# Kernel tuning notes

Measured on AMD Instinct MI355X. Metric: run time of the kernel, lower is better.

## Reference

```python
import jax, jax.numpy as jnp
import numpy as np

B, C, W, H = 4, 256, 64, 64
N = W * H
SCALE = 0.02  # keep QK^T energies in a stable softmax range


def setup_inputs() -> dict:
    key = jax.random.key(0)
    ks = jax.random.split(key, 8)
    return {
        "x": jax.random.normal(ks[0], (B, C, W, H), jnp.float32),
        "geo_embed": jax.random.normal(ks[1], (B, N, C), jnp.float32),
        "Wq": jax.random.normal(ks[2], (C, C), jnp.float32) * SCALE,
        "bq": jnp.zeros((C,), jnp.float32),
        "Wk": jax.random.normal(ks[3], (C, C), jnp.float32) * SCALE,
        "bk": jnp.zeros((C,), jnp.float32),
        "Wv": jax.random.normal(ks[4], (C, C), jnp.float32) * SCALE,
        "bv": jnp.zeros((C,), jnp.float32),
        "Wgp": jax.random.normal(ks[5], (C, C), jnp.float32) * SCALE,
        "bgp": jnp.zeros((C,), jnp.float32),
        "Wgg": jax.random.normal(ks[6], (1, 2 * C), jnp.float32) * SCALE,
        "bgg": jnp.zeros((1,), jnp.float32),
    }


def reference(x, geo_embed, Wq, bq, Wk, bk, Wv, bv, Wgp, bgp, Wgg, bgg):
    b, c, w, h = x.shape
    n = w * h
    xf = x.reshape(b, c, n)  # [B, C, N]

    # 1x1 conv == per-pixel linear; q laid out [B, N, O] (permuted in torch)
    q = jnp.einsum("oc,bcn->bno", Wq, xf) + bq  # [B, N, O]

    # geo gating on the query
    ge = geo_embed @ Wgp.T + bgp  # [B, N, O]
    gate = jax.nn.sigmoid(jnp.concatenate([q, ge], axis=-1) @ Wgg.T + bgg)  # [B, N, 1]
    q = q + gate * ge

    k = jnp.einsum("oc,bcn->bon", Wk, xf) + bk[:, None]  # [B, O, N]
    v = jnp.einsum("oc,bcn->bon", Wv, xf) + bv[:, None]  # [B, C, N]

    energy = jnp.einsum("bno,bom->bnm", q, k)  # [B, N, N]
    attention = jax.nn.softmax(energy, axis=-1)

    # out = bmm(value, attention^T): out[b,c,m] = sum_n v[b,c,n] * attention[b,m,n]
    out = jnp.einsum("bcn,bmn->bcm", v, attention).reshape(b, c, w, h)

    # output gating: torch .view reinterpretation of (B, N, O) as (B, C, W, H)
    ge_r = ge.reshape(b, c, w, h)
    out = out * (1.0 + jax.nn.sigmoid(ge_r))
    return out, attention
```

## Files before the change

kernel.cpp:

```cpp
#include <hip/hip_runtime.h>
#include <hip/hip_bf16.h>
#include <math.h>

static constexpr int BB = 4;
static constexpr int CC = 256;
static constexpr int NN = 4096;

using bf16   = __bf16;
using f16    = _Float16;
using bf16x8 = __attribute__((ext_vector_type(8))) __bf16;
using bf16x4 = __attribute__((ext_vector_type(4))) __bf16;
using f16x8  = __attribute__((ext_vector_type(8))) _Float16;
using f32x4  = __attribute__((ext_vector_type(4))) float;

__device__ inline void gload_lds16(const void* g, void* l) {
  __builtin_amdgcn_global_load_lds(
      (const __attribute__((address_space(1))) void*)g,
      (__attribute__((address_space(3))) void*)l, 16, 0, 0);
}

__device__ inline void swz_bid(int& xb, int& yb, int& zb) {
  int gx = gridDim.x, gy = gridDim.y;
  int nwg = gx * gy * (int)gridDim.z;
  int flat = blockIdx.x + gx * (blockIdx.y + gy * blockIdx.z);
  int q = nwg >> 3;
  int w = (flat & 7) * q + (flat >> 3);
  xb = w % gx;
  int r = w / gx;
  yb = r % gy;
  zb = r / gy;
}

__global__ __launch_bounds__(256) void cvt_weights_kernel(
    const float* __restrict__ w0, const float* __restrict__ w1,
    const float* __restrict__ w2, const float* __restrict__ w3,
    bf16* __restrict__ out) {
  const float* srcs[4] = {w0, w1, w2, w3};
  const float* s = srcs[blockIdx.y];
  bf16* dst = out + (size_t)blockIdx.y * (CC * CC);
  int i = (blockIdx.x * 256 + threadIdx.x) * 4;
  float4 v = *(const float4*)(s + i);
  bf16x4 t;
  t[0] = (bf16)v.x; t[1] = (bf16)v.y; t[2] = (bf16)v.z; t[3] = (bf16)v.w;
  *(bf16x4*)(dst + i) = t;
}

__global__ __launch_bounds__(256) void cvt_f32_bf16_kernel(
    const float* __restrict__ in, bf16* __restrict__ out, long n) {
  long i = ((long)blockIdx.x * blockDim.x + threadIdx.x) * 4;
  if (i >= n) return;
  float4 v = *(const float4*)(in + i);
  bf16x4 t;
  t[0] = (bf16)v.x; t[1] = (bf16)v.y; t[2] = (bf16)v.z; t[3] = (bf16)v.w;
  *(bf16x4*)(out + i) = t;
}

__global__ __launch_bounds__(256) void transpose_x_kernel(
    const float* __restrict__ x, bf16* __restrict__ xt) {
  __shared__ float tile[64][65];
  int b  = blockIdx.z;
  int c0 = blockIdx.x * 64;
  int n0 = blockIdx.y * 64;
  const float* xp = x  + (long)b * CC * NN;
  bf16*       xtp = xt + (long)b * NN * CC;
  int tj = threadIdx.x & 63;
  int ti = threadIdx.x >> 6;
#pragma unroll
  for (int p = 0; p < 16; ++p) {
    int i = ti + p * 4;
    tile[i][tj] = xp[(long)(c0 + i) * NN + n0 + tj];
  }
  __syncthreads();
#pragma unroll
  for (int p = 0; p < 16; ++p) {
    int i = ti + p * 4;
    xtp[(long)(n0 + i) * CC + c0 + tj] = (bf16)tile[tj][i];
  }
}

__global__ __launch_bounds__(256) void proj_all_kernel(
    const bf16* __restrict__ xt, const bf16* __restrict__ geob,
    const bf16* __restrict__ Wall,
    const float* __restrict__ bq, const float* __restrict__ bgp,
    const float* __restrict__ bk, const float* __restrict__ bv,
    bf16* __restrict__ qn, float* __restrict__ ge,
    bf16* __restrict__ kn, bf16* __restrict__ vb) {
  __shared__ bf16 As[128 * 32];
  __shared__ bf16 Bs[128 * 32];
  const long NCst = (long)NN * CC;
  const int bz = blockIdx.z;
  const int b = bz >> 2, p = bz & 3;
  const bf16 *Ap, *Bp;
  const float* bias;
  int row0, col0;
  if (p == 3) {
    Ap = Wall + 2 * CC * CC;
    Bp = xt + b * NCst;
    bias = bv;
    row0 = blockIdx.x * 128;
    col0 = blockIdx.y * 128;
  } else {
    Ap = (p == 1 ? geob : xt) + b * NCst;
    Bp = Wall + (size_t)(p == 0 ? 0 : (p == 1 ? 3 : 1)) * CC * CC;
    bias = (p == 0 ? bq : (p == 1 ? bgp : bk));
    row0 = blockIdx.y * 128;
    col0 = blockIdx.x * 128;
  }

  const int t   = threadIdx.x;
  const int wid = t >> 6;
  const int l   = t & 63;
  const int lr  = l & 15;
  const int lk  = (l >> 4) * 8;
  const int warow = (wid >> 1) * 64;
  const int wbcol = (wid & 1) * 64;
  const int srow = t >> 2;
  const int scol = (t & 3) * 8;

  f32x4 acc[4][4];
#pragma unroll
  for (int i = 0; i < 4; ++i)
#pragma unroll
    for (int j = 0; j < 4; ++j) acc[i][j] = {0.f, 0.f, 0.f, 0.f};

  for (int k0 = 0; k0 < CC; k0 += 32) {
    __syncthreads();
#pragma unroll
    for (int q = 0; q < 2; ++q)
      gload_lds16(Ap + (long)(row0 + srow + 64 * q) * CC + k0 + scol,
                  As + ((q * 256 + t) * 8));
#pragma unroll
    for (int q = 0; q < 2; ++q)
      gload_lds16(Bp + (long)(col0 + srow + 64 * q) * CC + k0 + scol,
                  Bs + ((q * 256 + t) * 8));
    __syncthreads();
    bf16x8 a[4], bb[4];
#pragma unroll
    for (int i = 0; i < 4; ++i)
      a[i] = *(const bf16x8*)(As + (warow + 16 * i + lr) * 32 + lk);
#pragma unroll
    for (int j = 0; j < 4; ++j)
      bb[j] = *(const bf16x8*)(Bs + (wbcol + 16 * j + lr) * 32 + lk);
#pragma unroll
    for (int i = 0; i < 4; ++i)
#pragma unroll
      for (int j = 0; j < 4; ++j)
        acc[i][j] = __builtin_amdgcn_mfma_f32_16x16x32_bf16(a[i], bb[j], acc[i][j], 0, 0, 0);
  }

  const int orow = (l >> 4) * 4;
  const int ocol = l & 15;
#pragma unroll
  for (int i = 0; i < 4; ++i) {
#pragma unroll
    for (int j = 0; j < 4; ++j) {
      int colb = col0 + wbcol + 16 * j + ocol;
#pragma unroll
      for (int r = 0; r < 4; ++r) {
        int row = row0 + warow + 16 * i + orow + r;
        if (p == 3) {
          float vv = acc[i][j][r] + bias[row];
          vb[b * NCst + (long)row * NN + colb] = (bf16)vv;
        } else {
          float vv = acc[i][j][r] + bias[colb];
          long di = b * NCst + (long)row * CC + colb;
          if (p == 1)
            ge[di] = vv;
          else
            (p == 0 ? qn : kn)[di] = (bf16)vv;
        }
      }
    }
  }
}

template <int BIAS_MODE, int B_MODE, int OUT_MODE, bool GATE_EPI, bool SWZ, bool STAT>
__global__ __launch_bounds__(256) void gemm_nt_lds(
    const bf16* __restrict__ A, const void* __restrict__ Bm,
    const float* __restrict__ bias, void* __restrict__ D,
    const float* __restrict__ gefl, float2* __restrict__ pstat,
    int Ncols, int K, long sA, long sB, long sD, long sGe) {
  __shared__ bf16 As[128 * 32];
  __shared__ bf16 Bs[128 * 32];
  int bx = blockIdx.x, by = blockIdx.y, bz = blockIdx.z;
  if constexpr (SWZ) swz_bid(bx, by, bz);
  const bf16* Ab = A + (long)bz * sA;
  const float* geb = GATE_EPI ? (gefl + bz * sGe) : nullptr;

  const int t   = threadIdx.x;
  const int wid = t >> 6;
  const int l   = t & 63;
  const int lr  = l & 15;
  const int lk  = (l >> 4) * 8;
  const int row0 = by * 128;
  const int col0 = bx * 128;
  const int warow = (wid >> 1) * 64;
  const int wbcol = (wid & 1) * 64;

  const int srow = t >> 2;
  const int scol = (t & 3) * 8;
  const int frow = t >> 3;
  const int fc4  = (t & 7) * 4;

  f32x4 acc[4][4];
#pragma unroll
  for (int i = 0; i < 4; ++i)
#pragma unroll
    for (int j = 0; j < 4; ++j) acc[i][j] = {0.f, 0.f, 0.f, 0.f};

  for (int k0 = 0; k0 < K; k0 += 32) {
    __syncthreads();
#pragma unroll
    for (int p = 0; p < 2; ++p)
      gload_lds16(Ab + (long)(row0 + srow + 64 * p) * K + k0 + scol,
                  As + ((p * 256 + t) * 8));
    if constexpr (B_MODE == 0) {
      const bf16* Bb = (const bf16*)Bm + (long)bz * sB;
#pragma unroll
      for (int p = 0; p < 2; ++p)
        gload_lds16(Bb + (long)(col0 + srow + 64 * p) * K + k0 + scol,
                    Bs + ((p * 256 + t) * 8));
    } else {
      const float* Bf = (const float*)Bm + (long)bz * sB;
#pragma unroll
      for (int p = 0; p < 4; ++p) {
        float4 u = *(const float4*)(Bf + (long)(col0 + frow + 32 * p) * K + k0 + fc4);
        bf16x4 tv;
        tv[0] = (bf16)u.x; tv[1] = (bf16)u.y; tv[2] = (bf16)u.z; tv[3] = (bf16)u.w;
        *(bf16x4*)(Bs + (frow + 32 * p) * 32 + fc4) = tv;
      }
    }
    __syncthreads();
    bf16x8 a[4], bb[4];
#pragma unroll
    for (int i = 0; i < 4; ++i)
      a[i] = *(const bf16x8*)(As + (warow + 16 * i + lr) * 32 + lk);
#pragma unroll
    for (int j = 0; j < 4; ++j)
      bb[j] = *(const bf16x8*)(Bs + (wbcol + 16 * j + lr) * 32 + lk);
#pragma unroll
    for (int i = 0; i < 4; ++i)
#pragma unroll
      for (int j = 0; j < 4; ++j)
        acc[i][j] = __builtin_amdgcn_mfma_f32_16x16x32_bf16(a[i], bb[j], acc[i][j], 0, 0, 0);
  }

  const int orow = (l >> 4) * 4;
  const int ocol = l & 15;
#pragma unroll
  for (int i = 0; i < 4; ++i) {
#pragma unroll
    for (int j = 0; j < 4; ++j) {
      int colb = col0 + wbcol + 16 * j + ocol;
#pragma unroll
      for (int r = 0; r < 4; ++r) {
        int row = row0 + warow + 16 * i + orow + r;
        float vv = acc[i][j][r];
        if constexpr (BIAS_MODE == 1) vv += bias[colb];
        if constexpr (BIAS_MODE == 2) vv += bias[row];
        if constexpr (GATE_EPI) {
          float g = geb[(long)row * 4096 + colb];
          vv *= 1.f + 1.f / (1.f + __expf(-g));
        }
        long di = bz * sD + (long)row * Ncols + colb;
        if constexpr (OUT_MODE == 0)
          ((float*)D)[di] = vv;
        else if constexpr (OUT_MODE == 1)
          ((bf16*)D)[di] = (bf16)vv;
        else
          ((f16*)D)[di] = (f16)vv;
      }
    }
  }

  if constexpr (STAT) {
    __shared__ float2 sm[128][2];
#pragma unroll
    for (int i = 0; i < 4; ++i) {
#pragma unroll
      for (int r = 0; r < 4; ++r) {
        float m = fmaxf(fmaxf(acc[i][0][r], acc[i][1][r]),
                        fmaxf(acc[i][2][r], acc[i][3][r]));
#pragma unroll
        for (int s = 8; s >= 1; s >>= 1) m = fmaxf(m, __shfl_xor(m, s, 64));
        float sum = 0.f;
#pragma unroll
        for (int j = 0; j < 4; ++j) sum += __expf(acc[i][j][r] - m);
#pragma unroll
        for (int s = 8; s >= 1; s >>= 1) sum += __shfl_xor(sum, s, 64);
        if ((l & 15) == 0) {
          int Rl = warow + 16 * i + (l >> 4) * 4 + r;
          sm[Rl][wid & 1] = make_float2(m, sum);
        }
      }
    }
    __syncthreads();
    if (t < 128) {
      float2 a2 = sm[t][0], b2 = sm[t][1];
      float m = fmaxf(a2.x, b2.x);
      float s = a2.y * __expf(a2.x - m) + b2.y * __expf(b2.x - m);
      pstat[((long)bz * NN + row0 + t) * 32 + bx] = make_float2(m, s);
    }
  }
}

__global__ __launch_bounds__(256) void rowstat_reduce_kernel(
    const float2* __restrict__ pstat, float2* __restrict__ minv) {
  int row = blockIdx.x * 4 + (threadIdx.x >> 6);
  int l = threadIdx.x & 63;
  float2 v = (l < 32) ? pstat[(long)row * 32 + l] : make_float2(-1e30f, 0.f);
  float m = v.x;
#pragma unroll
  for (int s = 16; s >= 1; s >>= 1) m = fmaxf(m, __shfl_xor(m, s, 64));
  float sum = v.y * __expf(v.x - m);
#pragma unroll
  for (int s = 16; s >= 1; s >>= 1) sum += __shfl_xor(sum, s, 64);
  if (l == 0) minv[row] = make_float2(m, 1.f / sum);
}

template <bool SWZ>
__global__ __launch_bounds__(512) void pv_fused_kernel(
    const bf16* __restrict__ V, const f16* __restrict__ E,
    const float2* __restrict__ minv, float* __restrict__ attn,
    float* __restrict__ out, const float* __restrict__ ge) {
  __shared__ bf16 Bs[2][64 * 64];
  int bx = blockIdx.x, by = blockIdx.y, bz = blockIdx.z;
  if constexpr (SWZ) swz_bid(bx, by, bz);
  const int mrow0 = bx * 64;
  const long NCst = (long)NN * CC;
  const long NNst = (long)NN * NN;
  const bf16* Vb = V + bz * NCst;
  const f16*  Eb = E + bz * NNst;
  float* attnb = attn + bz * NNst;
  const float* geb = ge + bz * NCst;
  float* ob = out + bz * NCst;

  const int t   = threadIdx.x;
  const int wid = t >> 6;
  const int l   = t & 63;
  const int lr  = l & 15;
  const int lk8 = l >> 4;
  const int crow = wid * 32;

  const int rE  = t >> 3;
  const int cE8 = (t & 7) * 8;
  const float2 mi = minv[(long)bz * NN + mrow0 + rE];
  const f16* Erow = Eb + (long)(mrow0 + rE) * NN + cE8;
  float* Arow = attnb + (long)(mrow0 + rE) * NN + cE8;
  const int bs_woff = rE * 64 + (((t & 7) ^ (rE & 7)) * 8);

  const bf16* Vr0 = Vb + (long)(crow + lr) * NN + lk8 * 8;
  const bf16* Vr1 = Vb + (long)(crow + 16 + lr) * NN + lk8 * 8;

  f32x4 acc[2][4];
#pragma unroll
  for (int i = 0; i < 2; ++i)
#pragma unroll
    for (int j = 0; j < 4; ++j) acc[i][j] = {0.f, 0.f, 0.f, 0.f};

  f16x8 ecur = *(const f16x8*)(Erow);

  auto produce = [&](int kdst, int buf) {
    float pv[8];
#pragma unroll
    for (int i = 0; i < 8; ++i) pv[i] = __expf((float)ecur[i] - mi.x) * mi.y;
    float4 u0 = {pv[0], pv[1], pv[2], pv[3]};
    float4 u1 = {pv[4], pv[5], pv[6], pv[7]};
    *(float4*)(Arow + kdst)     = u0;
    *(float4*)(Arow + kdst + 4) = u1;
    bf16x8 pb;
#pragma unroll
    for (int i = 0; i < 8; ++i) pb[i] = (bf16)pv[i];
    *(bf16x8*)(&Bs[buf][bs_woff]) = pb;
    ecur = *(const f16x8*)(Erow + ((kdst + 64) & (NN - 1)));
  };

  auto consume = [&](int buf, bf16x8 a00, bf16x8 a01, bf16x8 a10, bf16x8 a11) {
    const bf16* B0 = &Bs[buf][0];
#pragma unroll
    for (int j = 0; j < 4; ++j) {
      int Rb = 16 * j + lr;
      bf16x8 b0 = *(const bf16x8*)(B0 + Rb * 64 + ((lk8 ^ (Rb & 7)) * 8));
      bf16x8 b1 = *(const bf16x8*)(B0 + Rb * 64 + (((lk8 + 4) ^ (Rb & 7)) * 8));
      acc[0][j] = __builtin_amdgcn_mfma_f32_16x16x32_bf16(a00, b0, acc[0][j], 0, 0, 0);
      acc[1][j] = __builtin_amdgcn_mfma_f32_16x16x32_bf16(a10, b0, acc[1][j], 0, 0, 0);
      acc[0][j] = __builtin_amdgcn_mfma_f32_16x16x32_bf16(a01, b1, acc[0][j], 0, 0, 0);
      acc[1][j] = __builtin_amdgcn_mfma_f32_16x16x32_bf16(a11, b1, acc[1][j], 0, 0, 0);
    }
  };

#define LOADV(k0, A0, A1, A2, A3)                  \
  A0 = *(const bf16x8*)(Vr0 + (k0));               \
  A1 = *(const bf16x8*)(Vr0 + (k0) + 32);          \
  A2 = *(const bf16x8*)(Vr1 + (k0));               \
  A3 = *(const bf16x8*)(Vr1 + (k0) + 32);

#define FENCE_BAR()                                         \
  asm volatile("s_waitcnt lgkmcnt(0)" ::: "memory");        \
  __builtin_amdgcn_s_barrier();                             \
  __builtin_amdgcn_sched_barrier(0);

  bf16x8 A00, A01, A10, A11, B00, B01, B10, B11;

  produce(0, 0);
  LOADV(0, A00, A01, A10, A11);
  FENCE_BAR();

  for (int it = 0; it < 31; ++it) {
    int k0 = it * 128;
    LOADV(k0 + 64, B00, B01, B10, B11);
    consume(0, A00, A01, A10, A11);
    produce(k0 + 64, 1);
    FENCE_BAR();
    LOADV(k0 + 128, A00, A01, A10, A11);
    consume(1, B00, B01, B10, B11);
    produce(k0 + 128, 0);
    FENCE_BAR();
  }
  LOADV(4032, B00, B01, B10, B11);
  consume(0, A00, A01, A10, A11);
  produce(4032, 1);
  FENCE_BAR();
  consume(1, B00, B01, B10, B11);
#undef LOADV
#undef FENCE_BAR

  const int orow = (l >> 4) * 4;
  const int ocol = l & 15;
#pragma unroll
  for (int i = 0; i < 2; ++i) {
#pragma unroll
    for (int j = 0; j < 4; ++j) {
      int m = mrow0 + 16 * j + ocol;
#pragma unroll
      for (int r = 0; r < 4; ++r) {
        int c = crow + 16 * i + orow + r;
        float g = geb[(long)c * 4096 + m];
        float vv = acc[i][j][r] * (1.f + 1.f / (1.f + __expf(-g)));
        ob[(long)c * 4096 + m] = vv;
      }
    }
  }
}

__global__ __launch_bounds__(256) void gate_kernel(
    bf16* __restrict__ q, const float* __restrict__ ge,
    const float* __restrict__ Wgg, const float* __restrict__ bgg) {
  int row = blockIdx.x * 4 + (threadIdx.x >> 6);
  int l = threadIdx.x & 63;
  bf16* qr = q + (long)row * 256;
  const float* ger = ge + (long)row * 256;
  float s = 0.f;
  float qv[4], gv[4];
#pragma unroll
  for (int i = 0; i < 4; ++i) {
    int o = l + 64 * i;
    qv[i] = (float)qr[o];
    gv[i] = ger[o];
    s += qv[i] * Wgg[o] + gv[i] * Wgg[256 + o];
  }
#pragma unroll
  for (int m = 32; m >= 1; m >>= 1) s += __shfl_xor(s, m, 64);
  float gate = 1.f / (1.f + __expf(-(s + bgg[0])));
#pragma unroll
  for (int i = 0; i < 4; ++i) {
    int o = l + 64 * i;
    qr[o] = (bf16)(qv[i] + gate * gv[i]);
  }
}

__global__ __launch_bounds__(256) void softmax32_kernel(float* __restrict__ attn) {
  long row = blockIdx.x;
  float* p = attn + row * 4096;
  int t = threadIdx.x;
  __shared__ float red[8];
  float4 v[4];
  float mx = -1e30f;
#pragma unroll
  for (int c = 0; c < 4; ++c) {
    v[c] = *(const float4*)(p + c * 1024 + t * 4);
    mx = fmaxf(mx, fmaxf(fmaxf(v[c].x, v[c].y), fmaxf(v[c].z, v[c].w)));
  }
#pragma unroll
  for (int m = 32; m >= 1; m >>= 1) mx = fmaxf(mx, __shfl_xor(mx, m, 64));
  if ((t & 63) == 0) red[t >> 6] = mx;
  __syncthreads();
  mx = fmaxf(fmaxf(red[0], red[1]), fmaxf(red[2], red[3]));
  float sum = 0.f;
#pragma unroll
  for (int c = 0; c < 4; ++c) {
    v[c].x = __expf(v[c].x - mx);
    v[c].y = __expf(v[c].y - mx);
    v[c].z = __expf(v[c].z - mx);
    v[c].w = __expf(v[c].w - mx);
    sum += v[c].x + v[c].y + v[c].z + v[c].w;
  }
#pragma unroll
  for (int m = 32; m >= 1; m >>= 1) sum += __shfl_xor(sum, m, 64);
  if ((t & 63) == 0) red[4 + (t >> 6)] = sum;
  __syncthreads();
  float inv = 1.f / (red[4] + red[5] + red[6] + red[7]);
#pragma unroll
  for (int c = 0; c < 4; ++c) {
    v[c].x *= inv; v[c].y *= inv; v[c].z *= inv; v[c].w *= inv;
    *(float4*)(p + c * 1024 + t * 4) = v[c];
  }
}

extern "C" void kernel_launch(void* const* d_in, const int* in_sizes, int n_in,
                              void* d_out, int out_size, void* d_ws, size_t ws_size,
                              hipStream_t stream) {
  const float* x    = (const float*)d_in[0];
  const float* geo  = (const float*)d_in[1];
  const float* Wq   = (const float*)d_in[2];
  const float* bq   = (const float*)d_in[3];
  const float* Wk   = (const float*)d_in[4];
  const float* bk   = (const float*)d_in[5];
  const float* Wv   = (const float*)d_in[6];
  const float* bv   = (const float*)d_in[7];
  const float* Wgp  = (const float*)d_in[8];
  const float* bgp  = (const float*)d_in[9];
  const float* Wgg  = (const float*)d_in[10];
  const float* bgg  = (const float*)d_in[11];

  float* out  = (float*)d_out;
  float* attn = out + (long)BB * CC * NN;

  char* w = (char*)d_ws;
  size_t used = 0;
  auto alloc = [&](size_t bytes) {
    char* p = w + used;
    used += (bytes + 255) & ~(size_t)255;
    return p;
  };
  bf16*  xt   = (bf16*)alloc((size_t)BB * NN * CC * 2);
  bf16*  geob = (bf16*)alloc((size_t)BB * NN * CC * 2);
  bf16*  qn   = (bf16*)alloc((size_t)BB * NN * CC * 2);
  bf16*  kn   = (bf16*)alloc((size_t)BB * NN * CC * 2);
  bf16*  vb   = (bf16*)alloc((size_t)BB * CC * NN * 2);
  float* ge   = (float*)alloc((size_t)BB * NN * CC * 4);
  bf16*  Wall = (bf16*)alloc((size_t)4 * CC * CC * 2);
  bf16*  Wvb  = Wall + 2 * CC * CC;
  size_t abf_bytes   = (size_t)BB * NN * NN * 2;
  size_t pstat_bytes = (size_t)BB * NN * 32 * sizeof(float2);
  size_t minv_bytes  = (size_t)BB * NN * sizeof(float2);
  bool big = (ws_size >= used + abf_bytes + pstat_bytes + minv_bytes + 1024);
  f16* abf = nullptr;
  float2* pstat = nullptr;
  float2* minv = nullptr;
  if (big) {
    abf   = (f16*)alloc(abf_bytes);
    pstat = (float2*)alloc(pstat_bytes);
    minv  = (float2*)alloc(minv_bytes);
  }

  const long NCst = (long)NN * CC;
  const long NNst = (long)NN * NN;

  cvt_weights_kernel<<<dim3(64, 4), 256, 0, stream>>>(Wq, Wk, Wv, Wgp, Wall);
  cvt_f32_bf16_kernel<<<(BB * NCst) / 1024, 256, 0, stream>>>(geo, geob, BB * NCst);
  transpose_x_kernel<<<dim3(4, 64, BB), 256, 0, stream>>>(x, xt);

  proj_all_kernel<<<dim3(2, 32, BB * 4), 256, 0, stream>>>(
      xt, geob, Wall, bq, bgp, bk, bv, qn, ge, kn, vb);
  gate_kernel<<<(BB * NN) / 4, 256, 0, stream>>>(qn, ge, Wgg, bgg);

  if (big) {
    gemm_nt_lds<0, 0, 2, false, true, true><<<dim3(32, 32, BB), 256, 0, stream>>>(
        qn, kn, nullptr, abf, nullptr, pstat, NN, CC, NCst, NCst, NNst, 0);
    rowstat_reduce_kernel<<<(BB * NN) / 4, 256, 0, stream>>>(pstat, minv);
    pv_fused_kernel<true><<<dim3(64, 1, BB), 512, 0, stream>>>(
        vb, abf, minv, attn, out, ge);
  } else {
    gemm_nt_lds<0, 0, 0, false, true, false><<<dim3(32, 32, BB), 256, 0, stream>>>(
        qn, kn, nullptr, attn, nullptr, nullptr, NN, CC, NCst, NCst, NNst, 0);
    softmax32_kernel<<<BB * NN, 256, 0, stream>>>(attn);
    gemm_nt_lds<0, 1, 0, true, true, false><<<dim3(32, 2, BB), 256, 0, stream>>>(
        vb, attn, nullptr, out, ge, nullptr, NN, NN, NCst, NNst, NCst, NCst);
  }
}
```

Baseline: 309.0 us.

## Split PV reduction over two K halves with a separate combine-and-gate kernel

The fused softmax-normalise/PV kernel now runs a grid twice as large, each block covering half of the key dimension and writing fp32 partial outputs to a workspace buffer. A new combine kernel adds the two partials and applies the sigmoid output gate. Each thread's E reads and attention writes are also reshaped into two 4-wide chunks spaced 32 apart instead of one 8-wide chunk. The point is to fill more CUs, since the old grid of 256 blocks underused the device. The cost is an extra launch plus 32 MB of partial-sum writes and reads.

```diff
diff --git a/kernel.cpp b/kernel.cpp
--- a/kernel.cpp
+++ b/kernel.cpp
@@ -11,6 +11,7 @@
 using bf16x8 = __attribute__((ext_vector_type(8))) __bf16;
 using bf16x4 = __attribute__((ext_vector_type(4))) __bf16;
 using f16x8  = __attribute__((ext_vector_type(8))) _Float16;
+using f16x4  = __attribute__((ext_vector_type(4))) _Float16;
 using f32x4  = __attribute__((ext_vector_type(4))) float;
 
 __device__ inline void gload_lds16(const void* g, void* l) {
@@ -322,18 +323,18 @@
 __global__ __launch_bounds__(512) void pv_fused_kernel(
     const bf16* __restrict__ V, const f16* __restrict__ E,
     const float2* __restrict__ minv, float* __restrict__ attn,
-    float* __restrict__ out, const float* __restrict__ ge) {
+    float* __restrict__ pbuf) {
   __shared__ bf16 Bs[2][64 * 64];
   int bx = blockIdx.x, by = blockIdx.y, bz = blockIdx.z;
   if constexpr (SWZ) swz_bid(bx, by, bz);
   const int mrow0 = bx * 64;
+  const int KBASE = by * (NN / 2);
   const long NCst = (long)NN * CC;
   const long NNst = (long)NN * NN;
   const bf16* Vb = V + bz * NCst;
   const f16*  Eb = E + bz * NNst;
   float* attnb = attn + bz * NNst;
-  const float* geb = ge + bz * NCst;
-  float* ob = out + bz * NCst;
+  float* pb = pbuf + (long)(bz * 2 + by) * NCst;
 
   const int t   = threadIdx.x;
   const int wid = t >> 6;
@@ -342,12 +343,15 @@
   const int lk8 = l >> 4;
   const int crow = wid * 32;
 
-  const int rE  = t >> 3;
-  const int cE8 = (t & 7) * 8;
+  const int rE = t >> 3;
+  const int q4 = (t & 7) * 4;
   const float2 mi = minv[(long)bz * NN + mrow0 + rE];
-  const f16* Erow = Eb + (long)(mrow0 + rE) * NN + cE8;
-  float* Arow = attnb + (long)(mrow0 + rE) * NN + cE8;
-  const int bs_woff = rE * 64 + (((t & 7) ^ (rE & 7)) * 8);
+  const f16* Erow = Eb + (long)(mrow0 + rE) * NN + q4;
+  float* Arow = attnb + (long)(mrow0 + rE) * NN + q4;
+  const int c8a = (t & 7) >> 1;
+  const int o4  = (t & 1) * 4;
+  const int woff1 = rE * 64 + ((c8a ^ (rE & 7)) << 3) + o4;
+  const int woff2 = rE * 64 + (((c8a + 4) ^ (rE & 7)) << 3) + o4;
 
   const bf16* Vr0 = Vb + (long)(crow + lr) * NN + lk8 * 8;
   const bf16* Vr1 = Vb + (long)(crow + 16 + lr) * NN + lk8 * 8;
@@ -358,21 +362,27 @@
 #pragma unroll
     for (int j = 0; j < 4; ++j) acc[i][j] = {0.f, 0.f, 0.f, 0.f};
 
-  f16x8 ecur = *(const f16x8*)(Erow);
+  f16x4 elo = *(const f16x4*)(Erow + KBASE);
+  f16x4 ehi = *(const f16x4*)(Erow + KBASE + 32);
 
   auto produce = [&](int kdst, int buf) {
-    float pv[8];
-#pragma unroll
-    for (int i = 0; i < 8; ++i) pv[i] = __expf((float)ecur[i] - mi.x) * mi.y;
-    float4 u0 = {pv[0], pv[1], pv[2], pv[3]};
-    float4 u1 = {pv[4], pv[5], pv[6], pv[7]};
-    *(float4*)(Arow + kdst)     = u0;
-    *(float4*)(Arow + kdst + 4) = u1;
-    bf16x8 pb;
-#pragma unroll
-    for (int i = 0; i < 8; ++i) pb[i] = (bf16)pv[i];
-    *(bf16x8*)(&Bs[buf][bs_woff]) = pb;
-    ecur = *(const f16x8*)(Erow + ((kdst + 64) & (NN - 1)));
+    float pl[4], ph[4];
+#pragma unroll
+    for (int i = 0; i < 4; ++i) pl[i] = __expf((float)elo[i] - mi.x) * mi.y;
+#pragma unroll
+    for (int i = 0; i < 4; ++i) ph[i] = __expf((float)ehi[i] - mi.x) * mi.y;
+    float4 u0 = {pl[0], pl[1], pl[2], pl[3]};
+    float4 u1 = {ph[0], ph[1], ph[2], ph[3]};
+    *(float4*)(Arow + kdst)      = u0;
+    *(float4*)(Arow + kdst + 32) = u1;
+    bf16x4 b0, b1;
+#pragma unroll
+    for (int i = 0; i < 4; ++i) { b0[i] = (bf16)pl[i]; b1[i] = (bf16)ph[i]; }
+    *(bf16x4*)(&Bs[buf][woff1]) = b0;
+    *(bf16x4*)(&Bs[buf][woff2]) = b1;
+    int kn = (kdst + 64) & (NN - 1);
+    elo = *(const f16x4*)(Erow + kn);
+    ehi = *(const f16x4*)(Erow + kn + 32);
   };
 
   auto consume = [&](int buf, bf16x8 a00, bf16x8 a01, bf16x8 a10, bf16x8 a11) {
@@ -402,12 +412,12 @@
 
   bf16x8 A00, A01, A10, A11, B00, B01, B10, B11;
 
-  produce(0, 0);
-  LOADV(0, A00, A01, A10, A11);
+  produce(KBASE, 0);
+  LOADV(KBASE, A00, A01, A10, A11);
   FENCE_BAR();
 
-  for (int it = 0; it < 31; ++it) {
-    int k0 = it * 128;
+  for (int it = 0; it < 15; ++it) {
+    int k0 = KBASE + it * 128;
     LOADV(k0 + 64, B00, B01, B10, B11);
     consume(0, A00, A01, A10, A11);
     produce(k0 + 64, 1);
@@ -417,9 +427,9 @@
     produce(k0 + 128, 0);
     FENCE_BAR();
   }
-  LOADV(4032, B00, B01, B10, B11);
+  LOADV(KBASE + 1984, B00, B01, B10, B11);
   consume(0, A00, A01, A10, A11);
-  produce(4032, 1);
+  produce(KBASE + 1984, 1);
   FENCE_BAR();
   consume(1, B00, B01, B10, B11);
 #undef LOADV
@@ -435,11 +445,34 @@
 #pragma unroll
       for (int r = 0; r < 4; ++r) {
         int c = crow + 16 * i + orow + r;
-        float g = geb[(long)c * 4096 + m];
-        float vv = acc[i][j][r] * (1.f + 1.f / (1.f + __expf(-g)));
-        ob[(long)c * 4096 + m] = vv;
+        pb[(long)c * 4096 + m] = acc[i][j][r];
       }
     }
+  }
+}
+
+__global__ __launch_bounds__(256) void combine_kernel(
+    const float* __restrict__ pbuf, const float* __restrict__ ge,
+    float* __restrict__ out) {
+  const long NCst = (long)NN * CC;
+  long i = ((long)blockIdx.x * 256 + threadIdx.x) * 8;
+  int b = (int)(i >> 20);
+  long r = i & (NCst - 1);
+  const float* p0 = pbuf + (long)(b * 2) * NCst + r;
+  const float* p1 = p0 + NCst;
+  const float* g  = ge + (long)b * NCst + r;
+  float* o = out + i;
+#pragma unroll
+  for (int h = 0; h < 2; ++h) {
+    float4 a = *(const float4*)(p0 + h * 4);
+    float4 c = *(const float4*)(p1 + h * 4);
+    float4 gv = *(const float4*)(g + h * 4);
+    float4 u;
+    u.x = (a.x + c.x) * (1.f + 1.f / (1.f + __expf(-gv.x)));
+    u.y = (a.y + c.y) * (1.f + 1.f / (1.f + __expf(-gv.y)));
+    u.z = (a.z + c.z) * (1.f + 1.f / (1.f + __expf(-gv.z)));
+    u.w = (a.w + c.w) * (1.f + 1.f / (1.f + __expf(-gv.w)));
+    *(float4*)(o + h * 4) = u;
   }
 }
 
@@ -544,14 +577,18 @@
   size_t abf_bytes   = (size_t)BB * NN * NN * 2;
   size_t pstat_bytes = (size_t)BB * NN * 32 * sizeof(float2);
   size_t minv_bytes  = (size_t)BB * NN * sizeof(float2);
-  bool big = (ws_size >= used + abf_bytes + pstat_bytes + minv_bytes + 1024);
+  size_t pbuf_bytes  = (size_t)BB * 2 * NN * CC * 4;
+  bool big = (ws_size >=
+              used + abf_bytes + pstat_bytes + minv_bytes + pbuf_bytes + 2048);
   f16* abf = nullptr;
   float2* pstat = nullptr;
   float2* minv = nullptr;
+  float* pbuf = nullptr;
   if (big) {
     abf   = (f16*)alloc(abf_bytes);
     pstat = (float2*)alloc(pstat_bytes);
     minv  = (float2*)alloc(minv_bytes);
+    pbuf  = (float*)alloc(pbuf_bytes);
   }
 
   const long NCst = (long)NN * CC;
@@ -569,8 +606,10 @@
     gemm_nt_lds<0, 0, 2, false, true, true><<<dim3(32, 32, BB), 256, 0, stream>>>(
         qn, kn, nullptr, abf, nullptr, pstat, NN, CC, NCst, NCst, NNst, 0);
     rowstat_reduce_kernel<<<(BB * NN) / 4, 256, 0, stream>>>(pstat, minv);
-    pv_fused_kernel<true><<<dim3(64, 1, BB), 512, 0, stream>>>(
-        vb, abf, minv, attn, out, ge);
+    pv_fused_kernel<true><<<dim3(64, 2, BB), 512, 0, stream>>>(
+        vb, abf, minv, attn, pbuf);
+    combine_kernel<<<(int)((long)BB * NCst / (256 * 8)), 256, 0, stream>>>(
+        pbuf, ge, out);
   } else {
     gemm_nt_lds<0, 0, 0, false, true, false><<<dim3(32, 32, BB), 256, 0, stream>>>(
         qn, kn, nullptr, attn, nullptr, nullptr, NN, CC, NCst, NCst, NNst, 0);
```

After: 300.3 us. 1.03x faster.
